# Optimization experiments

Measured on AMD Instinct MI355X. Metric: run time of the kernel, lower is better.

The kernel has to match this reference:

```python
import jax, jax.numpy as jnp
import numpy as np
import math

IN_C, N_EMBD, HEADS = 256, 512, 8

def setup_inputs() -> dict:
    key = jax.random.key(0)
    ks = jax.random.split(key, 5)
    B, T = 64, 500
    x = jax.random.normal(ks[0], (B, T, IN_C), dtype=jnp.float32)
    # torch Linear: y = x @ W.T + b; store W as [out, in]
    w_attn = jax.random.normal(ks[1], (3 * N_EMBD, IN_C), dtype=jnp.float32) * (1.0 / math.sqrt(IN_C))
    b_attn = jax.random.normal(ks[2], (3 * N_EMBD,), dtype=jnp.float32) * 0.02
    w_proj = jax.random.normal(ks[3], (N_EMBD, N_EMBD), dtype=jnp.float32) * (1.0 / math.sqrt(N_EMBD))
    b_proj = jax.random.normal(ks[4], (N_EMBD,), dtype=jnp.float32) * 0.02
    return {"x": x, "w_attn": w_attn, "b_attn": b_attn, "w_proj": w_proj, "b_proj": b_proj}

def reference(x, w_attn, b_attn, w_proj, b_proj):
    B, T, C = x.shape
    H, D = HEADS, N_EMBD // HEADS
    qkv = jnp.einsum('btc,ec->bte', x, w_attn) + b_attn  # [B,T,3*n_embd]
    q, k, v = jnp.split(qkv, 3, axis=-1)
    # [B,T,n_embd] -> [B,H,T,D]
    q = q.reshape(B, T, H, D).transpose(0, 2, 1, 3)
    k = k.reshape(B, T, H, D).transpose(0, 2, 1, 3)
    v = v.reshape(B, T, H, D).transpose(0, 2, 1, 3)
    att = jnp.einsum('bhtd,bhsd->bhts', q, k) * (1.0 / math.sqrt(D))
    # bias buffer is all-ones: masked_fill(bias==0, -inf) is a no-op
    att = jax.nn.softmax(att, axis=-1)
    y = jnp.einsum('bhts,bhsd->bhtd', att, v)  # [B,H,T,D]
    y = y.transpose(0, 2, 1, 3).reshape(B, T, N_EMBD)
    return jnp.einsum('bte,fe->btf', y, w_proj) + b_proj
```

## Files before the change

### kernel.cpp

```cpp
#include <hip/hip_runtime.h>

typedef _Float16 f16;
typedef _Float16 f16x8 __attribute__((ext_vector_type(8)));
typedef _Float16 f16x4 __attribute__((ext_vector_type(4)));
typedef _Float16 f16x2 __attribute__((ext_vector_type(2)));
typedef float    f32x16 __attribute__((ext_vector_type(16)));
typedef unsigned int u32;

typedef const __attribute__((address_space(1))) void GVOID;
typedef __attribute__((address_space(3))) void LVOID;

static __device__ __forceinline__ f32x16 mfma32(f16x8 a, f16x8 b, f32x16 c) {
  return __builtin_amdgcn_mfma_f32_32x32x16_f16(a, b, c, 0, 0, 0);
}
static __device__ __forceinline__ void gl_lds16(const f16* g, f16* l) {
  __builtin_amdgcn_global_load_lds((GVOID*)g, (LVOID*)l, 16, 0, 0);
}
static __device__ __forceinline__ u32 pk(float a, float b) {
  union { f16x2 h; u32 w; } u;
  u.h[0] = (f16)a; u.h[1] = (f16)b;
  return u.w;
}
static __device__ __forceinline__ u32 pkh(f16 a, f16 b) {
  union { f16x2 h; u32 w; } u;
  u.h[0] = a; u.h[1] = b;
  return u.w;
}
static __device__ __forceinline__ f16x8 mkfrag(float a0, float a1, float a2, float a3,
                                               float a4, float a5, float a6, float a7) {
  u32 c01 = pk(a0, a1), c23 = pk(a2, a3), c45 = pk(a4, a5), c67 = pk(a6, a7);
  asm("v_permlane32_swap_b32 %0, %1" : "+v"(c01), "+v"(c45));
  asm("v_permlane32_swap_b32 %0, %1" : "+v"(c23), "+v"(c67));
  union { f16x8 h; u32 w[4]; } u;
  u.w[0] = c01; u.w[1] = c23; u.w[2] = c45; u.w[3] = c67;
  return u.h;
}

__global__ __launch_bounds__(256)
void cvt_all(const float* __restrict__ x,  f16* __restrict__ xh,
             const float* __restrict__ wa, f16* __restrict__ wah,
             const float* __restrict__ wp, f16* __restrict__ wph) {
  int i = (blockIdx.x * 256 + threadIdx.x) * 8;
  const float* s; f16* d;
  if (i < 8192000)            { s = x + i;                 d = xh + i; }
  else if (i < 8192000+393216){ int j = i - 8192000;       s = wa + j; d = wah + j; }
  else                        { int j = i - 8585216;       s = wp + j; d = wph + j; }
  float4 v0 = *(const float4*)(s);
  float4 v1 = *(const float4*)(s + 4);
  f16x8 h;
  h[0] = (f16)v0.x; h[1] = (f16)v0.y; h[2] = (f16)v0.z; h[3] = (f16)v0.w;
  h[4] = (f16)v1.x; h[5] = (f16)v1.y; h[6] = (f16)v1.z; h[7] = (f16)v1.w;
  *(f16x8*)d = h;
}

template<int EPI, int KD, int NDIM>
__global__ __launch_bounds__(512)
void gemm8p(const f16* __restrict__ A, const f16* __restrict__ B,
            const float* __restrict__ bias, f16* __restrict__ outH,
            float* __restrict__ outF) {
  constexpr int KT = KD / 64;
  constexpr int ABUF = 256 * 64, BBUF = 128 * 64, BUFSZ = ABUF + BBUF;
  __shared__ __align__(16) f16 lds[3 * BUFSZ];

  const int nwg = gridDim.x, orig = blockIdx.x;
  const int xcd = orig & 7, loc = orig >> 3;
  const int qq = nwg >> 3, rr8 = nwg & 7;
  const int gb = (xcd < rr8 ? xcd * (qq + 1) : rr8 * (qq + 1) + (xcd - rr8) * qq) + loc;
  constexpr int NB = NDIM / 128;
  const int mb = gb / NB, nb = gb - mb * NB;
  const int m0 = mb * 256, n0 = nb * 128;

  const int tid = threadIdx.x, wid = tid >> 6;
  const int l31 = tid & 31, hi = (tid >> 5) & 1;
  const int wm = (wid >> 2) * 128, wn = (wid & 3) * 32;

  f32x16 acc[4] = {};

  auto STAGE = [&](int t) {
    const int k0 = t * 64;
    f16* Ab = &lds[(t % 3) * BUFSZ];
    f16* Bb = Ab + ABUF;
#pragma unroll
    for (int i = 0; i < 4; ++i) {
      int c = i * 512 + tid, row = c >> 3;
      int col = 8 * ((c & 7) ^ (row & 7));
      gl_lds16(A + (size_t)(m0 + row) * KD + k0 + col, &Ab[c * 8]);
    }
#pragma unroll
    for (int i = 0; i < 2; ++i) {
      int c = i * 512 + tid, row = c >> 3;
      int col = 8 * ((c & 7) ^ (row & 7));
      gl_lds16(B + (size_t)(n0 + row) * KD + k0 + col, &Bb[c * 8]);
    }
  };

  STAGE(0);
  STAGE(1);

#pragma unroll
  for (int t = 0; t < KT; ++t) {
    if (t + 2 < KT) STAGE(t + 2);
    if (t < KT - 2)       asm volatile("s_waitcnt vmcnt(12)" ::: "memory");
    else if (t == KT - 2) asm volatile("s_waitcnt vmcnt(6)"  ::: "memory");
    else                  asm volatile("s_waitcnt vmcnt(0)"  ::: "memory");
    __builtin_amdgcn_sched_barrier(0);
    __builtin_amdgcn_s_barrier();
    __builtin_amdgcn_sched_barrier(0);

    const f16* Ab = &lds[(t % 3) * BUFSZ];
    const f16* Bb = Ab + ABUF;
#pragma unroll
    for (int kk = 0; kk < 4; ++kk) {
      f16x8 af[4], bf;
      {
        int rb = wn + l31;
        bf = *(const f16x8*)&Bb[rb * 64 + 8 * ((2 * kk + hi) ^ (rb & 7))];
      }
#pragma unroll
      for (int ms = 0; ms < 4; ++ms) {
        int ra = wm + ms * 32 + l31;
        af[ms] = *(const f16x8*)&Ab[ra * 64 + 8 * ((2 * kk + hi) ^ (ra & 7))];
      }
      __builtin_amdgcn_sched_barrier(0);
      __builtin_amdgcn_s_barrier();
      __builtin_amdgcn_sched_barrier(0);
      __builtin_amdgcn_s_setprio(1);
#pragma unroll
      for (int ms = 0; ms < 4; ++ms)
        acc[ms] = mfma32(af[ms], bf, acc[ms]);
      __builtin_amdgcn_s_setprio(0);
      __builtin_amdgcn_sched_barrier(0);
      __builtin_amdgcn_s_barrier();
      __builtin_amdgcn_sched_barrier(0);
    }
  }

  float bv = bias[n0 + wn + l31];
#pragma unroll
  for (int ms = 0; ms < 4; ++ms)
#pragma unroll
    for (int r = 0; r < 16; ++r) {
      int mrow = (r & 3) + 8 * (r >> 2) + 4 * hi;
      int m_g = m0 + wm + ms * 32 + mrow;
      int n_g = n0 + wn + l31;
      float v = acc[ms][r] + bv;
      if (EPI == 0) outH[(size_t)m_g * NDIM + n_g] = (f16)v;
      else          outF[(size_t)m_g * NDIM + n_g] = v;
    }
}

__global__ __launch_bounds__(512, 4)
void attn_kern(const f16* __restrict__ qkv, f16* __restrict__ Yg) {
  __shared__ __align__(16) f16 Kl[2][64 * 64];
  __shared__ __align__(16) f16 VT[2][64 * 64];
  const int id = blockIdx.x;
  const int g = (id & 7) * 128 + (id >> 3);
  const int bh = g >> 1, qt = g & 1;
  const int b = bh >> 3, h = bh & 7;
  const int tid = threadIdx.x, w = tid >> 6;
  const int l31 = tid & 31, hi = (tid & 63) >> 5, e7 = l31 & 7;

  const f16* base  = qkv + (size_t)b * 500 * 1536 + h * 64;
  const f16* Kbase = base + 512;
  const f16* Vbase = base + 1024;

  const int q = qt * 256 + w * 32 + l31;
  const int qc = q < 500 ? q : 499;
  f16x8 qf[4];
  const f16* qp = base + (size_t)qc * 1536 + hi * 8;
#pragma unroll
  for (int ds = 0; ds < 4; ++ds) qf[ds] = *(const f16x8*)(qp + 16 * ds);
  const f16 qs = (f16)(0.125f * 1.44269504f);
#pragma unroll
  for (int ds = 0; ds < 4; ++ds)
#pragma unroll
    for (int j = 0; j < 8; ++j) qf[ds][j] *= qs;

  f32x16 O0 = {}, O1 = {};
  float l = 0.f;

  const int krow = tid >> 3, kcol = 8 * ((tid & 7) ^ (krow & 7));
  const int kvp = (tid & 31) * 2, d4 = (tid >> 5) * 4;
  f16x4 va, vb;
  const f16x4 VZ4 = {};

  {
    gl_lds16(Kbase + (size_t)krow * 1536 + kcol, &Kl[0][tid * 8]);
    const f16* vp0 = Vbase + (size_t)kvp * 1536 + d4;
    va = *(const f16x4*)vp0; vb = *(const f16x4*)(vp0 + 1536);
#pragma unroll
    for (int dd = 0; dd < 4; ++dd) {
      int d = d4 + dd;
      *(u32*)&VT[0][d * 64 + (kvp ^ ((d & 7) << 3))] = pkh(va[dd], vb[dd]);
    }
    __syncthreads();
  }

#pragma unroll 2
  for (int kt = 0; kt < 8; ++kt) {
    const int cur = kt & 1, nxt = cur ^ 1;
    if (kt < 7) {
      const int kvn = (kt + 1) * 64;
      int kr = kvn + krow; kr = kr < 500 ? kr : 499;
      gl_lds16(Kbase + (size_t)kr * 1536 + kcol, &Kl[nxt][tid * 8]);
      int kv = kvn + kvp;
      int kc0 = kv < 500 ? kv : 499, kc1 = kv + 1 < 500 ? kv + 1 : 499;
      va = *(const f16x4*)(Vbase + (size_t)kc0 * 1536 + d4);
      vb = *(const f16x4*)(Vbase + (size_t)kc1 * 1536 + d4);
      if (kv >= 500) va = VZ4;
      if (kv + 1 >= 500) vb = VZ4;
    }

    f32x16 s0 = {}, s1 = {};
    __builtin_amdgcn_s_setprio(1);
#pragma unroll
    for (int ds = 0; ds < 4; ++ds) {
      f16x8 k0 = *(const f16x8*)&Kl[cur][l31 * 64 + 8 * ((hi + 2 * ds) ^ e7)];
      f16x8 k1 = *(const f16x8*)&Kl[cur][(32 + l31) * 64 + 8 * ((hi + 2 * ds) ^ e7)];
      s0 = mfma32(k0, qf[ds], s0);
      s1 = mfma32(k1, qf[ds], s1);
    }
    __builtin_amdgcn_s_setprio(0);

    if (kt == 7) {
#pragma unroll
      for (int r = 0; r < 16; ++r) {
        int kvL = (r & 3) + 8 * (r >> 2) + 4 * hi;
        if (480 + kvL >= 500) s1[r] = -1e30f;
      }
    }

    float ps = 0.f;
#pragma unroll
    for (int r = 0; r < 16; ++r) {
      float t = __builtin_amdgcn_exp2f(s0[r]);
      s0[r] = t; ps += t;
    }
#pragma unroll
    for (int r = 0; r < 16; ++r) {
      float t = __builtin_amdgcn_exp2f(s1[r]);
      s1[r] = t; ps += t;
    }
    ps += __shfl_xor(ps, 32);
    l += ps;

    f16x8 pf0 = mkfrag(s0[0], s0[1], s0[2], s0[3], s0[4], s0[5], s0[6], s0[7]);
    f16x8 pf1 = mkfrag(s0[8], s0[9], s0[10], s0[11], s0[12], s0[13], s0[14], s0[15]);
    f16x8 pf2 = mkfrag(s1[0], s1[1], s1[2], s1[3], s1[4], s1[5], s1[6], s1[7]);
    f16x8 pf3 = mkfrag(s1[8], s1[9], s1[10], s1[11], s1[12], s1[13], s1[14], s1[15]);

    __builtin_amdgcn_s_setprio(1);
#pragma unroll
    for (int ks = 0; ks < 4; ++ks) {
      f16x8 pf = ks == 0 ? pf0 : ks == 1 ? pf1 : ks == 2 ? pf2 : pf3;
      int sw = (16 * ks + 8 * hi) ^ (e7 << 3);
      f16x8 v0 = *(const f16x8*)&VT[cur][l31 * 64 + sw];
      f16x8 v1 = *(const f16x8*)&VT[cur][(32 + l31) * 64 + sw];
      O0 = mfma32(pf, v0, O0);
      O1 = mfma32(pf, v1, O1);
    }
    __builtin_amdgcn_s_setprio(0);

    if (kt < 7) {
#pragma unroll
      for (int dd = 0; dd < 4; ++dd) {
        int d = d4 + dd;
        *(u32*)&VT[nxt][d * 64 + (kvp ^ ((d & 7) << 3))] = pkh(va[dd], vb[dd]);
      }
    }
    __syncthreads();
  }

  float linv = __builtin_amdgcn_rcpf(l);
#pragma unroll
  for (int r = 0; r < 16; ++r) {
    int rowv = (r & 3) + 8 * (r >> 2) + 4 * hi;
    float li = __shfl(linv, rowv);
    int t = qt * 256 + w * 32 + rowv;
    if (t < 500) {
      size_t rowb = (size_t)(b * 500 + t) * 512 + h * 64;
      Yg[rowb + l31]      = (f16)(O0[r] * li);
      Yg[rowb + 32 + l31] = (f16)(O1[r] * li);
    }
  }
}

extern "C" void kernel_launch(void* const* d_in, const int* in_sizes, int n_in,
                              void* d_out, int out_size, void* d_ws, size_t ws_size,
                              hipStream_t stream) {
  const float* x      = (const float*)d_in[0];
  const float* w_attn = (const float*)d_in[1];
  const float* b_attn = (const float*)d_in[2];
  const float* w_proj = (const float*)d_in[3];
  const float* b_proj = (const float*)d_in[4];
  float* out = (float*)d_out;

  char* wsp = (char*)d_ws;
  f16* Yg   = (f16*)wsp;
  f16* x_h  = (f16*)wsp;
  f16* qkv  = (f16*)(wsp + 32768000);
  f16* wa_h = (f16*)(wsp + 32768000 + 98304000);
  f16* wp_h = (f16*)(wsp + 32768000 + 98304000 + 786432);
  if (ws_size < 132382720) return;

  cvt_all<<<4320, dim3(256), 0, stream>>>(x, x_h, w_attn, wa_h, w_proj, wp_h);

  gemm8p<0, 256, 1536><<<1500, dim3(512), 0, stream>>>(x_h, wa_h, b_attn, qkv, nullptr);
  attn_kern<<<1024, dim3(512), 0, stream>>>(qkv, Yg);
  gemm8p<1, 512, 512><<<500, dim3(512), 0, stream>>>(Yg, wp_h, b_proj, nullptr, out);
}
```

Baseline: 142.6 us.

## Shrink GEMM tiles to 128x128 with double buffering and fewer barriers

Replaces the 256x128 triple-buffered GEMM with a 128x128 double-buffered version and doubles the grid sizes for both projections. The per-kk barriers around the MFMA groups are removed, leaving one barrier at the start and end of each K step. This cuts LDS use and raises occupancy and wave-level parallelism, which matters most for the small 500-block output projection. The cost is less operand reuse per tile and shallower prefetch, so latency is hidden less well.

Result: faster. 137.7 us (-3.4%).

```diff
diff --git a/kernel.cpp b/kernel.cpp
--- a/kernel.cpp
+++ b/kernel.cpp
@@ -55,12 +55,12 @@
 
 template<int EPI, int KD, int NDIM>
 __global__ __launch_bounds__(512)
-void gemm8p(const f16* __restrict__ A, const f16* __restrict__ B,
+void gemmdb(const f16* __restrict__ A, const f16* __restrict__ B,
             const float* __restrict__ bias, f16* __restrict__ outH,
             float* __restrict__ outF) {
   constexpr int KT = KD / 64;
-  constexpr int ABUF = 256 * 64, BBUF = 128 * 64, BUFSZ = ABUF + BBUF;
-  __shared__ __align__(16) f16 lds[3 * BUFSZ];
+  constexpr int ABUF = 128 * 64, BUFSZ = 2 * ABUF;
+  __shared__ __align__(16) f16 lds[2 * BUFSZ];
 
   const int nwg = gridDim.x, orig = blockIdx.x;
   const int xcd = orig & 7, loc = orig >> 3;
@@ -68,76 +68,62 @@
   const int gb = (xcd < rr8 ? xcd * (qq + 1) : rr8 * (qq + 1) + (xcd - rr8) * qq) + loc;
   constexpr int NB = NDIM / 128;
   const int mb = gb / NB, nb = gb - mb * NB;
-  const int m0 = mb * 256, n0 = nb * 128;
+  const int m0 = mb * 128, n0 = nb * 128;
 
   const int tid = threadIdx.x, wid = tid >> 6;
   const int l31 = tid & 31, hi = (tid >> 5) & 1;
-  const int wm = (wid >> 2) * 128, wn = (wid & 3) * 32;
-
-  f32x16 acc[4] = {};
-
-  auto STAGE = [&](int t) {
+  const int wm = (wid >> 2) * 64, wn = (wid & 3) * 32;
+
+  f32x16 acc[2] = {};
+
+  const int c0 = tid, c1 = 512 + tid;
+  const int r0 = c0 >> 3, col0 = 8 * ((c0 & 7) ^ (r0 & 7));
+  const int r1 = c1 >> 3, col1 = 8 * ((c1 & 7) ^ (r1 & 7));
+
+  auto STAGE = [&](int t, int bufi) {
     const int k0 = t * 64;
-    f16* Ab = &lds[(t % 3) * BUFSZ];
+    f16* Ab = &lds[bufi * BUFSZ];
     f16* Bb = Ab + ABUF;
-#pragma unroll
-    for (int i = 0; i < 4; ++i) {
-      int c = i * 512 + tid, row = c >> 3;
-      int col = 8 * ((c & 7) ^ (row & 7));
-      gl_lds16(A + (size_t)(m0 + row) * KD + k0 + col, &Ab[c * 8]);
-    }
-#pragma unroll
-    for (int i = 0; i < 2; ++i) {
-      int c = i * 512 + tid, row = c >> 3;
-      int col = 8 * ((c & 7) ^ (row & 7));
-      gl_lds16(B + (size_t)(n0 + row) * KD + k0 + col, &Bb[c * 8]);
-    }
+    gl_lds16(A + (size_t)(m0 + r0) * KD + k0 + col0, &Ab[c0 * 8]);
+    gl_lds16(A + (size_t)(m0 + r1) * KD + k0 + col1, &Ab[c1 * 8]);
+    gl_lds16(B + (size_t)(n0 + r0) * KD + k0 + col0, &Bb[c0 * 8]);
+    gl_lds16(B + (size_t)(n0 + r1) * KD + k0 + col1, &Bb[c1 * 8]);
   };
 
-  STAGE(0);
-  STAGE(1);
-
+  STAGE(0, 0);
+  int cur = 0;
 #pragma unroll
   for (int t = 0; t < KT; ++t) {
-    if (t + 2 < KT) STAGE(t + 2);
-    if (t < KT - 2)       asm volatile("s_waitcnt vmcnt(12)" ::: "memory");
-    else if (t == KT - 2) asm volatile("s_waitcnt vmcnt(6)"  ::: "memory");
-    else                  asm volatile("s_waitcnt vmcnt(0)"  ::: "memory");
+    if (t + 1 < KT) {
+      STAGE(t + 1, cur ^ 1);
+      asm volatile("s_waitcnt vmcnt(4)" ::: "memory");
+    } else {
+      asm volatile("s_waitcnt vmcnt(0)" ::: "memory");
+    }
     __builtin_amdgcn_sched_barrier(0);
     __builtin_amdgcn_s_barrier();
-    __builtin_amdgcn_sched_barrier(0);
-
-    const f16* Ab = &lds[(t % 3) * BUFSZ];
+
+    const f16* Ab = &lds[cur * BUFSZ];
     const f16* Bb = Ab + ABUF;
+    __builtin_amdgcn_s_setprio(1);
 #pragma unroll
     for (int kk = 0; kk < 4; ++kk) {
-      f16x8 af[4], bf;
-      {
-        int rb = wn + l31;
-        bf = *(const f16x8*)&Bb[rb * 64 + 8 * ((2 * kk + hi) ^ (rb & 7))];
-      }
-#pragma unroll
-      for (int ms = 0; ms < 4; ++ms) {
-        int ra = wm + ms * 32 + l31;
-        af[ms] = *(const f16x8*)&Ab[ra * 64 + 8 * ((2 * kk + hi) ^ (ra & 7))];
-      }
-      __builtin_amdgcn_sched_barrier(0);
-      __builtin_amdgcn_s_barrier();
-      __builtin_amdgcn_sched_barrier(0);
-      __builtin_amdgcn_s_setprio(1);
-#pragma unroll
-      for (int ms = 0; ms < 4; ++ms)
-        acc[ms] = mfma32(af[ms], bf, acc[ms]);
-      __builtin_amdgcn_s_setprio(0);
-      __builtin_amdgcn_sched_barrier(0);
-      __builtin_amdgcn_s_barrier();
-      __builtin_amdgcn_sched_barrier(0);
-    }
+      int rb = wn + l31;
+      f16x8 bf = *(const f16x8*)&Bb[rb * 64 + 8 * ((2 * kk + hi) ^ (rb & 7))];
+      int ra0 = wm + l31, ra1 = wm + 32 + l31;
+      f16x8 af0 = *(const f16x8*)&Ab[ra0 * 64 + 8 * ((2 * kk + hi) ^ (ra0 & 7))];
+      f16x8 af1 = *(const f16x8*)&Ab[ra1 * 64 + 8 * ((2 * kk + hi) ^ (ra1 & 7))];
+      acc[0] = mfma32(af0, bf, acc[0]);
+      acc[1] = mfma32(af1, bf, acc[1]);
+    }
+    __builtin_amdgcn_s_setprio(0);
+    __builtin_amdgcn_s_barrier();
+    cur ^= 1;
   }
 
   float bv = bias[n0 + wn + l31];
 #pragma unroll
-  for (int ms = 0; ms < 4; ++ms)
+  for (int ms = 0; ms < 2; ++ms)
 #pragma unroll
     for (int r = 0; r < 16; ++r) {
       int mrow = (r & 3) + 8 * (r >> 2) + 4 * hi;
@@ -305,7 +291,7 @@
 
   cvt_all<<<4320, dim3(256), 0, stream>>>(x, x_h, w_attn, wa_h, w_proj, wp_h);
 
-  gemm8p<0, 256, 1536><<<1500, dim3(512), 0, stream>>>(x_h, wa_h, b_attn, qkv, nullptr);
+  gemmdb<0, 256, 1536><<<3000, dim3(512), 0, stream>>>(x_h, wa_h, b_attn, qkv, nullptr);
   attn_kern<<<1024, dim3(512), 0, stream>>>(qkv, Yg);
-  gemm8p<1, 512, 512><<<500, dim3(512), 0, stream>>>(Yg, wp_h, b_proj, nullptr, out);
-}
+  gemmdb<1, 512, 512><<<1000, dim3(512), 0, stream>>>(Yg, wp_h, b_proj, nullptr, out);
+}
```
